# Optimization experiments

Measured on AMD Instinct MI355X. Metric: run time of the kernel, lower is better.

Reference implementation:

```python
import jax, jax.numpy as jnp
import numpy as np

DT = 0.1  # fixed dt offset from init_kwargs


def setup_inputs() -> dict:
    key = jax.random.key(0)
    ks = jax.random.split(key, 8)
    B_, L, D, N = 4, 4096, 128, 16
    s = 1.0 / np.sqrt(D)
    # S4D-Real init: A_n = -(n+1), repeated over input_dim (random_init=False)
    A = jnp.broadcast_to(-(jnp.arange(N, dtype=jnp.float32) + 1.0), (D, N))
    return {
        "x": jax.random.normal(ks[0], (B_, L, D), dtype=jnp.float32),
        "A": A,
        "Wb": jax.random.uniform(ks[1], (N, D), minval=-s, maxval=s, dtype=jnp.float32),
        "bb": jax.random.uniform(ks[2], (N,), minval=-s, maxval=s, dtype=jnp.float32),
        "Wc": jax.random.uniform(ks[3], (N, D), minval=-s, maxval=s, dtype=jnp.float32),
        "bc": jax.random.uniform(ks[4], (N,), minval=-s, maxval=s, dtype=jnp.float32),
        "Wd": jax.random.uniform(ks[5], (1, D), minval=-s, maxval=s, dtype=jnp.float32),
        "bd": jax.random.uniform(ks[6], (1,), minval=-s, maxval=s, dtype=jnp.float32),
    }


def reference(x, A, Wb, bb, Wc, bc, Wd, bd):
    # x: [B, L, D]; A: [D, N]
    Bp = x @ Wb.T + bb                                   # [B, L, N]  (self.sb)
    C = x @ Wc.T + bc                                    # [B, L, N]  (self.sc)
    # DeltaNetwork: softplus(Linear(x)) + dt, repeated over input_dim
    delta = jax.nn.softplus(x @ Wd.T + bd) + DT          # [B, L, 1]
    delta = jnp.broadcast_to(delta, x.shape)             # [B, L, D]
    # discretize: A_bar = exp(dt*A); B_bar = (1 - exp(-dt*A)) * (dt x B)
    dA = delta[..., None] * A                            # [B, L, D, N]
    A_bar = jnp.exp(dA)
    Bx = (1.0 - jnp.exp(-dA)) * delta[..., None] * Bp[:, :, None, :] * x[..., None]  # B_bar * x_t

    def step(h, inp):
        A_t, Bx_t, C_t = inp                             # [B,D,N],[B,D,N],[B,N]
        h = A_t * h + Bx_t
        y_t = jnp.sum(h * C_t[:, None, :], axis=-1)      # [B, D]
        return h, y_t

    h0 = jnp.zeros((x.shape[0], x.shape[2], A.shape[1]), x.dtype)
    _, y = jax.lax.scan(
        step, h0,
        (A_bar.transpose(1, 0, 2, 3), Bx.transpose(1, 0, 2, 3), C.transpose(1, 0, 2)),
    )
    return y.transpose(1, 0, 2)                          # [B, L, D]
```

## Files before the change

### kernel.cpp

```cpp
#include <hip/hip_runtime.h>
#include <math.h>

#define B_ 4
#define L_ 4096
#define D_ 128
#define N_ 16
#define DT_ 0.1f
#define CH_ 64
#define NCH_ 64
#define MAGICF 0x5D5D5D5Du

#define HL_OFF 0
#define PR_OFF 524288
#define FL_OFF 528384

__global__ __launch_bounds__(512) void s6_fused(const float* __restrict__ x,
                                                const float* __restrict__ A,
                                                const float* __restrict__ Wb,
                                                const float* __restrict__ bb,
                                                const float* __restrict__ Wc,
                                                const float* __restrict__ bc,
                                                const float* __restrict__ Wd,
                                                const float* __restrict__ bd,
                                                float* __restrict__ ws,
                                                float* __restrict__ y) {
    __shared__ float xs[64][132];
    __shared__ float proj[64][36];
    __shared__ float delta_s[64];
    __shared__ float Ssum[64];
    __shared__ float a_s[64][16];
    __shared__ float c_s[64][16];
    __shared__ float C_s[64][16];
    __shared__ float w_s[64][16];
    __shared__ float ylocal[64][132];
    __shared__ float h0s[128][20];

    const int t = threadIdx.x;
    const int blk = blockIdx.x;
    const int b = blk >> 6;
    const int c = blk & 63;
    const size_t rowbase = (size_t)b * L_ + c * CH_;

    const float4* xg = (const float4*)(x + rowbase * 128);
#pragma unroll
    for (int i = t; i < 2048; i += 512) {
        float4 v = xg[i];
        int r = i >> 5, k4 = (i & 31) << 2;
        xs[r][k4] = v.x; xs[r][k4 + 1] = v.y;
        xs[r][k4 + 2] = v.z; xs[r][k4 + 3] = v.w;
    }
    __syncthreads();

    {
        const int q = __builtin_amdgcn_readfirstlane(t >> 6);
        const int r = t & 63;
        const float* wp = (q < 4) ? (Wb + (size_t)q * 4 * 128)
                                  : (Wc + (size_t)(q - 4) * 4 * 128);
        float a0 = 0.f, a1 = 0.f, a2 = 0.f, a3 = 0.f;
#pragma unroll 8
        for (int k4 = 0; k4 < 32; ++k4) {
            float4 xv = *(const float4*)&xs[r][k4 * 4];
            float4 w0 = *(const float4*)(wp + k4 * 4);
            float4 w1 = *(const float4*)(wp + 128 + k4 * 4);
            float4 w2 = *(const float4*)(wp + 256 + k4 * 4);
            float4 w3 = *(const float4*)(wp + 384 + k4 * 4);
            a0 = fmaf(xv.x, w0.x, a0); a0 = fmaf(xv.y, w0.y, a0);
            a0 = fmaf(xv.z, w0.z, a0); a0 = fmaf(xv.w, w0.w, a0);
            a1 = fmaf(xv.x, w1.x, a1); a1 = fmaf(xv.y, w1.y, a1);
            a1 = fmaf(xv.z, w1.z, a1); a1 = fmaf(xv.w, w1.w, a1);
            a2 = fmaf(xv.x, w2.x, a2); a2 = fmaf(xv.y, w2.y, a2);
            a2 = fmaf(xv.z, w2.z, a2); a2 = fmaf(xv.w, w2.w, a2);
            a3 = fmaf(xv.x, w3.x, a3); a3 = fmaf(xv.y, w3.y, a3);
            a3 = fmaf(xv.z, w3.z, a3); a3 = fmaf(xv.w, w3.w, a3);
        }
        proj[r][q * 4]     = a0;
        proj[r][q * 4 + 1] = a1;
        proj[r][q * 4 + 2] = a2;
        proj[r][q * 4 + 3] = a3;
        if (q == 0) {
            float ad = 0.f;
#pragma unroll 8
            for (int k4 = 0; k4 < 32; ++k4) {
                float4 xv = *(const float4*)&xs[r][k4 * 4];
                float4 wv = *(const float4*)(Wd + k4 * 4);
                ad = fmaf(xv.x, wv.x, ad); ad = fmaf(xv.y, wv.y, ad);
                ad = fmaf(xv.z, wv.z, ad); ad = fmaf(xv.w, wv.w, ad);
            }
            proj[r][32] = ad;
        }
    }
    __syncthreads();

    if (t < 64) {
        float z = proj[t][32] + bd[0];
        float sp = fmaxf(z, 0.f) + log1pf(expf(-fabsf(z)));
        float dl = sp + DT_;
        delta_s[t] = dl;
        float v = dl;
#pragma unroll
        for (int off = 1; off < 64; off <<= 1) {
            float u = __shfl_up(v, off);
            if (t >= off) v += u;
        }
        Ssum[t] = v;
    }
    __syncthreads();

#pragma unroll
    for (int p = t; p < 1024; p += 512) {
        int r = p >> 4, n = p & 15;
        float An = A[n];
        float dl = delta_s[r];
        float Bp = proj[r][n] + bb[n];
        float Cv = proj[r][16 + n] + bc[n];
        float dA = dl * An;
        a_s[r][n] = expf(dA);
        c_s[r][n] = (1.f - expf(-dA)) * dl * Bp;
        C_s[r][n] = Cv;
        w_s[r][n] = Cv * expf(An * Ssum[r]);
    }
    if (t < 16) ws[PR_OFF + (size_t)blk * 16 + t] = expf(A[t] * Ssum[63]);
    __syncthreads();

    if (t < 256) {
        const int d = t >> 1;
        const int nh = t & 1;
        const int n0 = nh << 3;
        float4 ha = {0.f, 0.f, 0.f, 0.f}, hb4 = {0.f, 0.f, 0.f, 0.f};
#pragma unroll 4
        for (int tt = 0; tt < 64; ++tt) {
            float4 a0 = *(const float4*)&a_s[tt][n0];
            float4 a1 = *(const float4*)&a_s[tt][n0 + 4];
            float4 c0 = *(const float4*)&c_s[tt][n0];
            float4 c1 = *(const float4*)&c_s[tt][n0 + 4];
            float4 C0 = *(const float4*)&C_s[tt][n0];
            float4 C1 = *(const float4*)&C_s[tt][n0 + 4];
            float xv = xs[tt][d];
            ha.x = fmaf(a0.x, ha.x, c0.x * xv);
            ha.y = fmaf(a0.y, ha.y, c0.y * xv);
            ha.z = fmaf(a0.z, ha.z, c0.z * xv);
            ha.w = fmaf(a0.w, ha.w, c0.w * xv);
            hb4.x = fmaf(a1.x, hb4.x, c1.x * xv);
            hb4.y = fmaf(a1.y, hb4.y, c1.y * xv);
            hb4.z = fmaf(a1.z, hb4.z, c1.z * xv);
            hb4.w = fmaf(a1.w, hb4.w, c1.w * xv);
            float yv = ha.x * C0.x;
            yv = fmaf(ha.y, C0.y, yv); yv = fmaf(ha.z, C0.z, yv);
            yv = fmaf(ha.w, C0.w, yv);
            yv = fmaf(hb4.x, C1.x, yv); yv = fmaf(hb4.y, C1.y, yv);
            yv = fmaf(hb4.z, C1.z, yv); yv = fmaf(hb4.w, C1.w, yv);
            yv += __shfl_xor(yv, 1);
            if (nh == 0) ylocal[tt][d] = yv;
        }
        float* hp = ws + HL_OFF + (size_t)blk * 2048 + d * 16 + n0;
        *(float4*)(hp)     = ha;
        *(float4*)(hp + 4) = hb4;
    }
    __syncthreads();

    unsigned* flg = (unsigned*)(ws + FL_OFF);
    if (t == 0) {
        __hip_atomic_store(&flg[blk], MAGICF, __ATOMIC_RELEASE,
                           __HIP_MEMORY_SCOPE_AGENT);
    }

    if (t < c) {
        int iter = 0;
        while (__hip_atomic_load(&flg[(b << 6) + t], __ATOMIC_RELAXED,
                                 __HIP_MEMORY_SCOPE_AGENT) != MAGICF) {
            __builtin_amdgcn_s_sleep(2);
            if (++iter > 50000000) break;
        }
    }
    __syncthreads();
    __threadfence();

    {
        const int d = t >> 2, nq = t & 3;
        float4 s = {0.f, 0.f, 0.f, 0.f};
        const float* hb = ws + HL_OFF + ((size_t)(b << 6)) * 2048 + d * 16 + nq * 4;
        const float* pb = ws + PR_OFF + ((size_t)(b << 6)) * 16 + nq * 4;
#pragma unroll 4
        for (int j = 0; j < c; ++j) {
            float4 hl = *(const float4*)(hb + (size_t)j * 2048);
            float4 p  = *(const float4*)(pb + (size_t)j * 16);
            s.x = fmaf(p.x, s.x, hl.x);
            s.y = fmaf(p.y, s.y, hl.y);
            s.z = fmaf(p.z, s.z, hl.z);
            s.w = fmaf(p.w, s.w, hl.w);
        }
        h0s[d][nq * 4]     = s.x;
        h0s[d][nq * 4 + 1] = s.y;
        h0s[d][nq * 4 + 2] = s.z;
        h0s[d][nq * 4 + 3] = s.w;
    }
    __syncthreads();

    {
        const int d2 = t & 127;
        const int rg = t >> 7;
        float4 ha = *(const float4*)&h0s[d2][0];
        float4 hb4 = *(const float4*)&h0s[d2][4];
        float4 hc4 = *(const float4*)&h0s[d2][8];
        float4 hd4 = *(const float4*)&h0s[d2][12];
        float* yo = y + (rowbase + rg * 16) * 128 + d2;
#pragma unroll
        for (int i = 0; i < 16; ++i) {
            int tt = rg * 16 + i;
            float4 wa = *(const float4*)&w_s[tt][0];
            float4 wb4 = *(const float4*)&w_s[tt][4];
            float4 wc4 = *(const float4*)&w_s[tt][8];
            float4 wd4 = *(const float4*)&w_s[tt][12];
            float s = ylocal[tt][d2];
            s = fmaf(wa.x, ha.x, s);   s = fmaf(wa.y, ha.y, s);
            s = fmaf(wa.z, ha.z, s);   s = fmaf(wa.w, ha.w, s);
            s = fmaf(wb4.x, hb4.x, s); s = fmaf(wb4.y, hb4.y, s);
            s = fmaf(wb4.z, hb4.z, s); s = fmaf(wb4.w, hb4.w, s);
            s = fmaf(wc4.x, hc4.x, s); s = fmaf(wc4.y, hc4.y, s);
            s = fmaf(wc4.z, hc4.z, s); s = fmaf(wc4.w, hc4.w, s);
            s = fmaf(wd4.x, hd4.x, s); s = fmaf(wd4.y, hd4.y, s);
            s = fmaf(wd4.z, hd4.z, s); s = fmaf(wd4.w, hd4.w, s);
            yo[i * 128] = s;
        }
    }
}

extern "C" void kernel_launch(void* const* d_in, const int* in_sizes, int n_in,
                              void* d_out, int out_size, void* d_ws, size_t ws_size,
                              hipStream_t stream) {
    const float* x  = (const float*)d_in[0];
    const float* A  = (const float*)d_in[1];
    const float* Wb = (const float*)d_in[2];
    const float* bb = (const float*)d_in[3];
    const float* Wc = (const float*)d_in[4];
    const float* bc = (const float*)d_in[5];
    const float* Wd = (const float*)d_in[6];
    const float* bd = (const float*)d_in[7];
    float* ws = (float*)d_ws;
    float* y  = (float*)d_out;

    s6_fused<<<256, 512, 0, stream>>>(x, A, Wb, bb, Wc, bc, Wd, bd, ws, y);
}
```

Measured before the change: 138.1 us.

## Split fused scan into three kernels replacing spin-wait inter-block sync

Replaces the single kernel, whose blocks spin on per-chunk flags, with three launches. The first computes the local chunk scans and writes partial y straight to the output. The second runs a sequential prefix combine of chunk-final states per (b,d,n). The third adds the carry-in contribution to y. It also remaps the local scan to use all 512 threads with 4 states each, and removes the O(c) serial combine that every block used to repeat. In exchange it pays extra launch overhead and a global round-trip of y and w through memory.

```diff
diff --git a/kernel.cpp b/kernel.cpp
--- a/kernel.cpp
+++ b/kernel.cpp
@@ -8,13 +8,14 @@
 #define DT_ 0.1f
 #define CH_ 64
 #define NCH_ 64
-#define MAGICF 0x5D5D5D5Du
+#define NBLK_ 256
 
 #define HL_OFF 0
-#define PR_OFF 524288
-#define FL_OFF 528384
-
-__global__ __launch_bounds__(512) void s6_fused(const float* __restrict__ x,
+#define H0_OFF 524288
+#define PR_OFF 1048576
+#define W_OFF  1052672
+
+__global__ __launch_bounds__(512) void kA_fused(const float* __restrict__ x,
                                                 const float* __restrict__ A,
                                                 const float* __restrict__ Wb,
                                                 const float* __restrict__ bb,
@@ -31,9 +32,6 @@
     __shared__ float a_s[64][16];
     __shared__ float c_s[64][16];
     __shared__ float C_s[64][16];
-    __shared__ float w_s[64][16];
-    __shared__ float ylocal[64][132];
-    __shared__ float h0s[128][20];
 
     const int t = threadIdx.x;
     const int blk = blockIdx.x;
@@ -106,122 +104,124 @@
     }
     __syncthreads();
 
+    {
+        float* wglob = ws + W_OFF + rowbase * 16;
 #pragma unroll
-    for (int p = t; p < 1024; p += 512) {
-        int r = p >> 4, n = p & 15;
-        float An = A[n];
-        float dl = delta_s[r];
-        float Bp = proj[r][n] + bb[n];
-        float Cv = proj[r][16 + n] + bc[n];
-        float dA = dl * An;
-        a_s[r][n] = expf(dA);
-        c_s[r][n] = (1.f - expf(-dA)) * dl * Bp;
-        C_s[r][n] = Cv;
-        w_s[r][n] = Cv * expf(An * Ssum[r]);
-    }
-    if (t < 16) ws[PR_OFF + (size_t)blk * 16 + t] = expf(A[t] * Ssum[63]);
-    __syncthreads();
-
-    if (t < 256) {
-        const int d = t >> 1;
-        const int nh = t & 1;
-        const int n0 = nh << 3;
-        float4 ha = {0.f, 0.f, 0.f, 0.f}, hb4 = {0.f, 0.f, 0.f, 0.f};
+        for (int p = t; p < 1024; p += 512) {
+            int r = p >> 4, n = p & 15;
+            float An = A[n];
+            float dl = delta_s[r];
+            float Bp = proj[r][n] + bb[n];
+            float Cv = proj[r][16 + n] + bc[n];
+            float dA = dl * An;
+            a_s[r][n] = expf(dA);
+            c_s[r][n] = (1.f - expf(-dA)) * dl * Bp;
+            C_s[r][n] = Cv;
+            wglob[p] = Cv * expf(An * Ssum[r]);
+        }
+        if (t < 16) ws[PR_OFF + (size_t)blk * 16 + t] = expf(A[t] * Ssum[63]);
+    }
+    __syncthreads();
+
+    {
+        const int w = t >> 6;
+        const int lane = t & 63;
+        const int ng = lane >> 4;
+        const int dq = lane & 15;
+        const int d = w * 16 + dq;
+        const int n0 = ng * 4;
+        float4 h = {0.f, 0.f, 0.f, 0.f};
+        float* yout = y + rowbase * 128 + d;
 #pragma unroll 4
         for (int tt = 0; tt < 64; ++tt) {
-            float4 a0 = *(const float4*)&a_s[tt][n0];
-            float4 a1 = *(const float4*)&a_s[tt][n0 + 4];
-            float4 c0 = *(const float4*)&c_s[tt][n0];
-            float4 c1 = *(const float4*)&c_s[tt][n0 + 4];
-            float4 C0 = *(const float4*)&C_s[tt][n0];
-            float4 C1 = *(const float4*)&C_s[tt][n0 + 4];
+            float4 a4 = *(const float4*)&a_s[tt][n0];
+            float4 c4 = *(const float4*)&c_s[tt][n0];
+            float4 C4 = *(const float4*)&C_s[tt][n0];
             float xv = xs[tt][d];
-            ha.x = fmaf(a0.x, ha.x, c0.x * xv);
-            ha.y = fmaf(a0.y, ha.y, c0.y * xv);
-            ha.z = fmaf(a0.z, ha.z, c0.z * xv);
-            ha.w = fmaf(a0.w, ha.w, c0.w * xv);
-            hb4.x = fmaf(a1.x, hb4.x, c1.x * xv);
-            hb4.y = fmaf(a1.y, hb4.y, c1.y * xv);
-            hb4.z = fmaf(a1.z, hb4.z, c1.z * xv);
-            hb4.w = fmaf(a1.w, hb4.w, c1.w * xv);
-            float yv = ha.x * C0.x;
-            yv = fmaf(ha.y, C0.y, yv); yv = fmaf(ha.z, C0.z, yv);
-            yv = fmaf(ha.w, C0.w, yv);
-            yv = fmaf(hb4.x, C1.x, yv); yv = fmaf(hb4.y, C1.y, yv);
-            yv = fmaf(hb4.z, C1.z, yv); yv = fmaf(hb4.w, C1.w, yv);
-            yv += __shfl_xor(yv, 1);
-            if (nh == 0) ylocal[tt][d] = yv;
+            h.x = fmaf(a4.x, h.x, c4.x * xv);
+            h.y = fmaf(a4.y, h.y, c4.y * xv);
+            h.z = fmaf(a4.z, h.z, c4.z * xv);
+            h.w = fmaf(a4.w, h.w, c4.w * xv);
+            float yv = h.x * C4.x;
+            yv = fmaf(h.y, C4.y, yv);
+            yv = fmaf(h.z, C4.z, yv);
+            yv = fmaf(h.w, C4.w, yv);
+            yv += __shfl_xor(yv, 16);
+            yv += __shfl_xor(yv, 32);
+            if (ng == 0) yout[tt * 128] = yv;
         }
         float* hp = ws + HL_OFF + (size_t)blk * 2048 + d * 16 + n0;
-        *(float4*)(hp)     = ha;
-        *(float4*)(hp + 4) = hb4;
-    }
-    __syncthreads();
-
-    unsigned* flg = (unsigned*)(ws + FL_OFF);
-    if (t == 0) {
-        __hip_atomic_store(&flg[blk], MAGICF, __ATOMIC_RELEASE,
-                           __HIP_MEMORY_SCOPE_AGENT);
-    }
-
-    if (t < c) {
-        int iter = 0;
-        while (__hip_atomic_load(&flg[(b << 6) + t], __ATOMIC_RELAXED,
-                                 __HIP_MEMORY_SCOPE_AGENT) != MAGICF) {
-            __builtin_amdgcn_s_sleep(2);
-            if (++iter > 50000000) break;
-        }
-    }
-    __syncthreads();
-    __threadfence();
-
-    {
-        const int d = t >> 2, nq = t & 3;
-        float4 s = {0.f, 0.f, 0.f, 0.f};
-        const float* hb = ws + HL_OFF + ((size_t)(b << 6)) * 2048 + d * 16 + nq * 4;
-        const float* pb = ws + PR_OFF + ((size_t)(b << 6)) * 16 + nq * 4;
+        *(float4*)hp = h;
+    }
+}
+
+__global__ __launch_bounds__(256, 4) void kB_combine(float* __restrict__ ws) {
+    const float* hL = ws + HL_OFF;
+    const float* Pp = ws + PR_OFF;
+    float* h0 = ws + H0_OFF;
+    const int tid = blockIdx.x * 256 + threadIdx.x;
+    const int b = tid >> 11;
+    const int dn = tid & 2047;
+    const int n = tid & 15;
+
+    const float* hp = hL + (size_t)(b * NCH_) * 2048 + dn;
+    const float* pp = Pp + (size_t)(b * NCH_) * 16 + n;
+    float* op = h0 + (size_t)(b * NCH_) * 2048 + dn;
+
+    float h = 0.f;
+    op[0] = 0.f;
+#pragma unroll 8
+    for (int j = 0; j < NCH_ - 1; ++j) {
+        float hl = hp[(size_t)j * 2048];
+        float p  = pp[(size_t)j * 16];
+        h = fmaf(p, h, hl);
+        op[(size_t)(j + 1) * 2048] = h;
+    }
+}
+
+__global__ __launch_bounds__(256, 4) void kC_update(const float* __restrict__ ws,
+                                                    float* __restrict__ y) {
+    __shared__ float w_s[64][16];
+    const int blk = blockIdx.x;
+    const int b = blk >> 6;
+    const int c = blk & 63;
+    const int t = threadIdx.x;
+    const size_t rowbase = (size_t)b * L_ + c * CH_;
+
+    {
+        float4 v = ((const float4*)(ws + W_OFF + rowbase * 16))[t];
+        int r = t >> 2, n0 = (t & 3) << 2;
+        w_s[r][n0] = v.x; w_s[r][n0 + 1] = v.y;
+        w_s[r][n0 + 2] = v.z; w_s[r][n0 + 3] = v.w;
+    }
+    __syncthreads();
+
+    const int d = t & 127;
+    const int rg = t >> 7;
+    const float* h0p = ws + H0_OFF + ((size_t)blk * 128 + d) * 16;
+    const float4 ha = *(const float4*)h0p;
+    const float4 hb = *(const float4*)(h0p + 4);
+    const float4 hc = *(const float4*)(h0p + 8);
+    const float4 hd = *(const float4*)(h0p + 12);
+
+    float* yp = y + (rowbase + rg * 32) * 128 + d;
 #pragma unroll 4
-        for (int j = 0; j < c; ++j) {
-            float4 hl = *(const float4*)(hb + (size_t)j * 2048);
-            float4 p  = *(const float4*)(pb + (size_t)j * 16);
-            s.x = fmaf(p.x, s.x, hl.x);
-            s.y = fmaf(p.y, s.y, hl.y);
-            s.z = fmaf(p.z, s.z, hl.z);
-            s.w = fmaf(p.w, s.w, hl.w);
-        }
-        h0s[d][nq * 4]     = s.x;
-        h0s[d][nq * 4 + 1] = s.y;
-        h0s[d][nq * 4 + 2] = s.z;
-        h0s[d][nq * 4 + 3] = s.w;
-    }
-    __syncthreads();
-
-    {
-        const int d2 = t & 127;
-        const int rg = t >> 7;
-        float4 ha = *(const float4*)&h0s[d2][0];
-        float4 hb4 = *(const float4*)&h0s[d2][4];
-        float4 hc4 = *(const float4*)&h0s[d2][8];
-        float4 hd4 = *(const float4*)&h0s[d2][12];
-        float* yo = y + (rowbase + rg * 16) * 128 + d2;
-#pragma unroll
-        for (int i = 0; i < 16; ++i) {
-            int tt = rg * 16 + i;
-            float4 wa = *(const float4*)&w_s[tt][0];
-            float4 wb4 = *(const float4*)&w_s[tt][4];
-            float4 wc4 = *(const float4*)&w_s[tt][8];
-            float4 wd4 = *(const float4*)&w_s[tt][12];
-            float s = ylocal[tt][d2];
-            s = fmaf(wa.x, ha.x, s);   s = fmaf(wa.y, ha.y, s);
-            s = fmaf(wa.z, ha.z, s);   s = fmaf(wa.w, ha.w, s);
-            s = fmaf(wb4.x, hb4.x, s); s = fmaf(wb4.y, hb4.y, s);
-            s = fmaf(wb4.z, hb4.z, s); s = fmaf(wb4.w, hb4.w, s);
-            s = fmaf(wc4.x, hc4.x, s); s = fmaf(wc4.y, hc4.y, s);
-            s = fmaf(wc4.z, hc4.z, s); s = fmaf(wc4.w, hc4.w, s);
-            s = fmaf(wd4.x, hd4.x, s); s = fmaf(wd4.y, hd4.y, s);
-            s = fmaf(wd4.z, hd4.z, s); s = fmaf(wd4.w, hd4.w, s);
-            yo[i * 128] = s;
-        }
+    for (int i = 0; i < 32; ++i) {
+        const int r = rg * 32 + i;
+        float4 wa = *(const float4*)&w_s[r][0];
+        float4 wb4 = *(const float4*)&w_s[r][4];
+        float4 wc4 = *(const float4*)&w_s[r][8];
+        float4 wd4 = *(const float4*)&w_s[r][12];
+        float s = yp[i * 128];
+        s = fmaf(wa.x, ha.x, s);   s = fmaf(wa.y, ha.y, s);
+        s = fmaf(wa.z, ha.z, s);   s = fmaf(wa.w, ha.w, s);
+        s = fmaf(wb4.x, hb.x, s);  s = fmaf(wb4.y, hb.y, s);
+        s = fmaf(wb4.z, hb.z, s);  s = fmaf(wb4.w, hb.w, s);
+        s = fmaf(wc4.x, hc.x, s);  s = fmaf(wc4.y, hc.y, s);
+        s = fmaf(wc4.z, hc.z, s);  s = fmaf(wc4.w, hc.w, s);
+        s = fmaf(wd4.x, hd.x, s);  s = fmaf(wd4.y, hd.y, s);
+        s = fmaf(wd4.z, hd.z, s);  s = fmaf(wd4.w, hd.w, s);
+        yp[i * 128] = s;
     }
 }
 
@@ -239,5 +239,7 @@
     float* ws = (float*)d_ws;
     float* y  = (float*)d_out;
 
-    s6_fused<<<256, 512, 0, stream>>>(x, A, Wb, bb, Wc, bc, Wd, bd, ws, y);
-}
+    kA_fused<<<256, 512, 0, stream>>>(x, A, Wb, bb, Wc, bc, Wd, bd, ws, y);
+    kB_combine<<<32, 256, 0, stream>>>(ws);
+    kC_update<<<256, 256, 0, stream>>>(ws, y);
+}
```

Measured after the change: 121.8 us. 1.13x faster.
